# Optimization experiments

Measured on AMD Instinct MI355X. Metric: run time of the kernel, lower is better.

The kernel has to match this reference:

```python
import jax, jax.numpy as jnp
import numpy as np


def setup_inputs() -> dict:
    key = jax.random.key(0)
    ks = jax.random.split(key, 6)
    B, L, X, Y, A = 128, 1024, 1024, 1024, 32
    stdv = 1.0 / np.sqrt(X)
    x = jax.random.normal(ks[0], (B, L, X), dtype=jnp.float32)
    y = jax.random.normal(ks[1], (B, Y), dtype=jnp.float32)
    x_mask = jax.random.randint(ks[2], (B, L), 0, 2).astype(bool)
    actions = jax.random.randint(ks[3], (B,), 0, A)
    weight = jax.random.uniform(ks[4], (A, Y, X), dtype=jnp.float32, minval=-stdv, maxval=stdv)
    bias = jax.random.uniform(ks[5], (A, X), dtype=jnp.float32, minval=-stdv, maxval=stdv)
    return {"x": x, "y": y, "x_mask": x_mask, "actions": actions, "weight": weight, "bias": bias}


def reference(x, y, x_mask, actions, weight, bias):
    # Gather per-sample action weight/bias (equivalent to one_hot @ weight.view trick)
    w = weight[actions]            # [B, Y, X]
    b = bias[actions]              # [B, X]
    Wy = jnp.einsum('by,byx->bx', y, w) + b   # [B, X]
    xWy = jnp.einsum('blx,bx->bl', x, Wy)     # [B, L]
    xWy = jnp.where(x_mask, -jnp.inf, xWy)
    # training mode -> log_softmax
    alpha = jax.nn.log_softmax(xWy, axis=-1)
    return alpha
```

## Files before the change

### kernel.cpp

```cpp
#include <hip/hip_runtime.h>
#include <math.h>

#define Bb 128
#define Ll 1024
#define Xx 1024
#define Yy 1024

#define NEG_BIG (-1e30f)

__global__ __launch_bounds__(256) void k_wy(
    const float* __restrict__ y, const int* __restrict__ actions,
    const float* __restrict__ weight, const float* __restrict__ bias,
    float* __restrict__ Wy)
{
    const int b  = blockIdx.y;
    const int x0 = (blockIdx.x * 256 + threadIdx.x) * 2;
    const int a  = actions[b];
    const float2* wp = (const float2*)(weight + (size_t)a * Yy * Xx + x0);
    const float*  yb = y + b * Yy;
    const float2  bv = *(const float2*)(bias + a * Xx + x0);
    float acc0 = bv.x, acc1 = bv.y;
#pragma unroll 8
    for (int yy = 0; yy < Yy; ++yy) {
        const float  yv = yb[yy];
        const float2 wv = wp[(size_t)yy * (Xx / 2)];
        acc0 += yv * wv.x;
        acc1 += yv * wv.y;
    }
    float2 o; o.x = acc0; o.y = acc1;
    *(float2*)(Wy + b * Xx + x0) = o;
}

__global__ __launch_bounds__(256) void k_dot(
    const float* __restrict__ x, const float* __restrict__ Wy,
    float* __restrict__ xWy)
{
    const int b    = blockIdx.y;
    const int lane = threadIdx.x & 63;
    const int wave = threadIdx.x >> 6;

    const float4* wy4 = (const float4*)(Wy + b * Xx);
    const float4 w0 = wy4[lane];
    const float4 w1 = wy4[64 + lane];
    const float4 w2 = wy4[128 + lane];
    const float4 w3 = wy4[192 + lane];

    const int lbase = blockIdx.x * 64 + wave * 16;
    const float4* xb = (const float4*)x + (size_t)b * Ll * 256;

#pragma unroll 2
    for (int i = 0; i < 16; ++i) {
        const int l = lbase + i;
        const float4* xr = xb + (size_t)l * 256;
        const float4 a0 = xr[lane];
        const float4 a1 = xr[64 + lane];
        const float4 a2 = xr[128 + lane];
        const float4 a3 = xr[192 + lane];
        float acc = a0.x * w0.x + a0.y * w0.y + a0.z * w0.z + a0.w * w0.w;
        acc      += a1.x * w1.x + a1.y * w1.y + a1.z * w1.z + a1.w * w1.w;
        acc      += a2.x * w2.x + a2.y * w2.y + a2.z * w2.z + a2.w * w2.w;
        acc      += a3.x * w3.x + a3.y * w3.y + a3.z * w3.z + a3.w * w3.w;
#pragma unroll
        for (int off = 32; off > 0; off >>= 1)
            acc += __shfl_xor(acc, off, 64);
        if (lane == 0) xWy[b * Ll + l] = acc;
    }
}

__global__ __launch_bounds__(256) void k_lsm(
    const float* __restrict__ xWy, const int* __restrict__ mask,
    float* __restrict__ out)
{
    const int b = blockIdx.x;
    const int t = threadIdx.x;
    const int lane = t & 63, wave = t >> 6;
    __shared__ float redm[4], reds[4];

    float v[4];
    float mx = NEG_BIG;
#pragma unroll
    for (int i = 0; i < 4; ++i) {
        const int l = t + i * 256;
        float val = xWy[b * Ll + l];
        if (mask[b * Ll + l] != 0) val = NEG_BIG;
        v[i] = val;
        mx = fmaxf(mx, val);
    }
#pragma unroll
    for (int off = 32; off > 0; off >>= 1)
        mx = fmaxf(mx, __shfl_xor(mx, off, 64));
    if (lane == 0) redm[wave] = mx;
    __syncthreads();
    mx = fmaxf(fmaxf(redm[0], redm[1]), fmaxf(redm[2], redm[3]));

    float s = 0.f;
#pragma unroll
    for (int i = 0; i < 4; ++i)
        s += expf(v[i] - mx);
#pragma unroll
    for (int off = 32; off > 0; off >>= 1)
        s += __shfl_xor(s, off, 64);
    if (lane == 0) reds[wave] = s;
    __syncthreads();
    s = reds[0] + reds[1] + reds[2] + reds[3];

    const float lse = mx + logf(s);
#pragma unroll
    for (int i = 0; i < 4; ++i)
        out[b * Ll + t + i * 256] = v[i] - lse;
}

extern "C" void kernel_launch(void* const* d_in, const int* in_sizes, int n_in,
                              void* d_out, int out_size, void* d_ws, size_t ws_size,
                              hipStream_t stream)
{
    const float* x       = (const float*)d_in[0];
    const float* y       = (const float*)d_in[1];
    const int*   x_mask  = (const int*)  d_in[2];
    const int*   actions = (const int*)  d_in[3];
    const float* weight  = (const float*)d_in[4];
    const float* bias    = (const float*)d_in[5];
    float* out = (float*)d_out;

    float* Wy  = (float*)d_ws;
    float* xWy = Wy + (size_t)Bb * Xx;

    k_wy <<<dim3(2, Bb),  256, 0, stream>>>(y, actions, weight, bias, Wy);
    k_dot<<<dim3(16, Bb), 256, 0, stream>>>(x, Wy, xWy);
    k_lsm<<<Bb,           256, 0, stream>>>(xWy, x_mask, out);
}
```

Baseline: 818.1 us.

## Group samples by action to reuse weight loads and split Y reduction

Adds a small grouping kernel that buckets batch samples by action into chunks of up to four. Each Wy block then loads a weight slice once and applies it to four samples. The Y dimension is also split in two, giving more blocks, and the partial sums are added inside the dot kernel. This is meant to cut redundant weight traffic and raise parallelism in the Wy stage, at the cost of an extra single-block launch and a serial grouping step.

```diff
diff --git a/kernel.cpp b/kernel.cpp
--- a/kernel.cpp
+++ b/kernel.cpp
@@ -5,45 +5,122 @@
 #define Ll 1024
 #define Xx 1024
 #define Yy 1024
+#define Aa 32
 
 #define NEG_BIG (-1e30f)
 
-__global__ __launch_bounds__(256) void k_wy(
-    const float* __restrict__ y, const int* __restrict__ actions,
-    const float* __restrict__ weight, const float* __restrict__ bias,
-    float* __restrict__ Wy)
-{
-    const int b  = blockIdx.y;
-    const int x0 = (blockIdx.x * 256 + threadIdx.x) * 2;
-    const int a  = actions[b];
-    const float2* wp = (const float2*)(weight + (size_t)a * Yy * Xx + x0);
-    const float*  yb = y + b * Yy;
-    const float2  bv = *(const float2*)(bias + a * Xx + x0);
-    float acc0 = bv.x, acc1 = bv.y;
+
+__global__ __launch_bounds__(128) void k_group(
+    const int* __restrict__ actions, int* __restrict__ meta)
+{
+    __shared__ int act[Bb];
+    __shared__ int cnt[Aa], start[Aa];
+    __shared__ int order[Bb];
+    const int t = threadIdx.x;
+    act[t] = actions[t];
+    if (t < Aa) cnt[t] = 0;
+    __syncthreads();
+    const int a = act[t];
+    int rank = 0;
+    for (int i = 0; i < t; ++i)
+        if (act[i] == a) rank++;
+    atomicAdd(&cnt[a], 1);
+    __syncthreads();
+    if (t == 0) {
+        int s = 0;
+        for (int i = 0; i < Aa; ++i) { start[i] = s; s += cnt[i]; }
+    }
+    __syncthreads();
+    order[start[a] + rank] = t;
+    __syncthreads();
+    if (t == 0) {
+        int nc = 0;
+        for (int i = 0; i < Aa; ++i) {
+            for (int j = 0; j < cnt[i]; j += 4) {
+                const int ns = min(4, cnt[i] - j);
+                meta[1 + nc]      = i;
+                meta[65 + nc]     = ns;
+                for (int k = 0; k < 4; ++k)
+                    meta[129 + nc * 4 + k] = order[start[i] + j + (k < ns ? k : 0)];
+                nc++;
+            }
+        }
+        meta[0] = nc;
+    }
+}
+
+__global__ __launch_bounds__(256) void k_wy2(
+    const float* __restrict__ y, const float* __restrict__ weight,
+    const float* __restrict__ bias, const int* __restrict__ meta,
+    float* __restrict__ part)
+{
+    const int c  = blockIdx.z;
+    if (c >= meta[0]) return;
+    const int a  = meta[1 + c];
+    const int ns = meta[65 + c];
+    const int s0 = meta[129 + c * 4 + 0];
+    const int s1 = meta[129 + c * 4 + 1];
+    const int s2 = meta[129 + c * 4 + 2];
+    const int s3 = meta[129 + c * 4 + 3];
+
+    const int hx = blockIdx.x;
+    const int hy = blockIdx.y;
+    const int x0 = hx * 512 + threadIdx.x * 2;
+    const int yb = hy * 512;
+
+    const float* y0 = y + s0 * Yy + yb;
+    const float* y1 = y + s1 * Yy + yb;
+    const float* y2 = y + s2 * Yy + yb;
+    const float* y3 = y + s3 * Yy + yb;
+    const float2* wp = (const float2*)(weight + (size_t)a * Yy * Xx
+                                              + (size_t)yb * Xx + x0);
+
+    float2 acc0, acc1, acc2, acc3;
+    if (hy == 0) {
+        const float2 bv = *(const float2*)(bias + a * Xx + x0);
+        acc0 = bv; acc1 = bv; acc2 = bv; acc3 = bv;
+    } else {
+        acc0 = {0.f, 0.f}; acc1 = acc0; acc2 = acc0; acc3 = acc0;
+    }
+
 #pragma unroll 8
-    for (int yy = 0; yy < Yy; ++yy) {
-        const float  yv = yb[yy];
+    for (int yy = 0; yy < 512; ++yy) {
         const float2 wv = wp[(size_t)yy * (Xx / 2)];
-        acc0 += yv * wv.x;
-        acc1 += yv * wv.y;
-    }
-    float2 o; o.x = acc0; o.y = acc1;
-    *(float2*)(Wy + b * Xx + x0) = o;
+        const float v0 = y0[yy], v1 = y1[yy], v2 = y2[yy], v3 = y3[yy];
+        acc0.x += v0 * wv.x; acc0.y += v0 * wv.y;
+        acc1.x += v1 * wv.x; acc1.y += v1 * wv.y;
+        acc2.x += v2 * wv.x; acc2.y += v2 * wv.y;
+        acc3.x += v3 * wv.x; acc3.y += v3 * wv.y;
+    }
+
+    float* pb = part + (size_t)hy * Bb * Xx;
+    *(float2*)(pb + (size_t)s0 * Xx + x0) = acc0;
+    if (ns > 1) *(float2*)(pb + (size_t)s1 * Xx + x0) = acc1;
+    if (ns > 2) *(float2*)(pb + (size_t)s2 * Xx + x0) = acc2;
+    if (ns > 3) *(float2*)(pb + (size_t)s3 * Xx + x0) = acc3;
 }
 
 __global__ __launch_bounds__(256) void k_dot(
-    const float* __restrict__ x, const float* __restrict__ Wy,
+    const float* __restrict__ x, const float* __restrict__ part,
     float* __restrict__ xWy)
 {
     const int b    = blockIdx.y;
     const int lane = threadIdx.x & 63;
     const int wave = threadIdx.x >> 6;
 
-    const float4* wy4 = (const float4*)(Wy + b * Xx);
-    const float4 w0 = wy4[lane];
-    const float4 w1 = wy4[64 + lane];
-    const float4 w2 = wy4[128 + lane];
-    const float4 w3 = wy4[192 + lane];
+    const float4* p0 = (const float4*)(part + (size_t)b * Xx);
+    const float4* p1 = (const float4*)(part + (size_t)(Bb + b) * Xx);
+    float4 w0, w1, w2, w3;
+    {
+        const float4 a0 = p0[lane],       b0 = p1[lane];
+        const float4 a1 = p0[64 + lane],  b1 = p1[64 + lane];
+        const float4 a2 = p0[128 + lane], b2 = p1[128 + lane];
+        const float4 a3 = p0[192 + lane], b3 = p1[192 + lane];
+        w0.x = a0.x + b0.x; w0.y = a0.y + b0.y; w0.z = a0.z + b0.z; w0.w = a0.w + b0.w;
+        w1.x = a1.x + b1.x; w1.y = a1.y + b1.y; w1.z = a1.z + b1.z; w1.w = a1.w + b1.w;
+        w2.x = a2.x + b2.x; w2.y = a2.y + b2.y; w2.z = a2.z + b2.z; w2.w = a2.w + b2.w;
+        w3.x = a3.x + b3.x; w3.y = a3.y + b3.y; w3.z = a3.z + b3.z; w3.w = a3.w + b3.w;
+    }
 
     const int lbase = blockIdx.x * 64 + wave * 16;
     const float4* xb = (const float4*)x + (size_t)b * Ll * 256;
@@ -122,10 +199,12 @@
     const float* bias    = (const float*)d_in[5];
     float* out = (float*)d_out;
 
-    float* Wy  = (float*)d_ws;
-    float* xWy = Wy + (size_t)Bb * Xx;
-
-    k_wy <<<dim3(2, Bb),  256, 0, stream>>>(y, actions, weight, bias, Wy);
-    k_dot<<<dim3(16, Bb), 256, 0, stream>>>(x, Wy, xWy);
-    k_lsm<<<Bb,           256, 0, stream>>>(xWy, x_mask, out);
-}
+    int*   meta = (int*)d_ws;
+    float* part = (float*)d_ws + 512;
+    float* xWy  = part + (size_t)2 * Bb * Xx;
+
+    k_group<<<1,               128, 0, stream>>>(actions, meta);
+    k_wy2  <<<dim3(2, 2, 64),  256, 0, stream>>>(y, weight, bias, meta, part);
+    k_dot  <<<dim3(16, Bb),    256, 0, stream>>>(x, part, xWy);
+    k_lsm  <<<Bb,              256, 0, stream>>>(xWy, x_mask, out);
+}
```

New measurement: 790.5 us. 3.4% less time.
